# Kernel optimization log

Measured on AMD Instinct MI355X. Metric: run time of the kernel, lower is better.

Reference implementation:

```python
import jax, jax.numpy as jnp
import numpy as np

B, H, T = 32, 80, 1600
C1, C2 = 32, 32
K, S, P = 3, 2, 1  # kernel, stride, padding on both dims


def setup_inputs() -> dict:
    key = jax.random.key(0)
    k1, k2, k3, k4, k5, k6 = jax.random.split(key, 6)
    inputs = jax.random.normal(k1, (B, 1, H, T), dtype=jnp.float32)
    seq_lengths = jax.random.randint(k2, (B,), 1, T + 1).astype(jnp.int32)
    W1 = jax.random.normal(k3, (C1, 1, K, K), dtype=jnp.float32) * 0.1
    b1 = jax.random.normal(k4, (C1,), dtype=jnp.float32) * 0.1
    W2 = jax.random.normal(k5, (C2, C1, K, K), dtype=jnp.float32) * 0.05
    b2 = jax.random.normal(k6, (C2,), dtype=jnp.float32) * 0.1
    return {"inputs": inputs, "seq_lengths": seq_lengths,
            "W1": W1, "b1": b1, "W2": W2, "b2": b2}


def _conv(x, W, b):
    y = jax.lax.conv_general_dilated(
        x, W, window_strides=(S, S), padding=((P, P), (P, P)),
        dimension_numbers=("NCHW", "OIHW", "NCHW"))
    return y + b[None, :, None, None]


def _new_lengths(L):
    # floor((L + 2p - d*(k-1) - 1)/s) + 1, matching _get_sequence_lengths
    return (L + 2 * P - (K - 1) - 1) // S + 1


def _mask_time(x, L):
    # zero positions t >= L[b] along the last (time) axis
    t = jnp.arange(x.shape[3])
    valid = (t[None, :] < L[:, None]).astype(x.dtype)  # [B, Tout]
    return x * valid[:, None, None, :]


def reference(inputs, seq_lengths, W1, b1, W2, b2):
    # conv1 + mask
    x = _conv(inputs, W1, b1)
    L = _new_lengths(seq_lengths)
    x = _mask_time(x, L)
    # relu + mask (lengths unchanged)
    x = _mask_time(jax.nn.relu(x), L)
    # conv2 + mask
    x = _conv(x, W2, b2)
    L = _new_lengths(L)
    x = _mask_time(x, L)
    # relu + mask
    x = _mask_time(jax.nn.relu(x), L)
    return x, L
```

## Files before the change

### kernel.cpp

```cpp
#include <hip/hip_runtime.h>
#include <hip/hip_bf16.h>

#define B_    32
#define H_IN  80
#define T_IN  1600
#define C1_   32
#define H1_   40
#define T1_   800
#define C2_   32
#define H2_   20
#define T2_   400

#define TH2   2
#define TT2   32
#define NH1   5
#define NT1   65
#define NIDX  33
#define RROWS 11
#define RCOLSW 66
#define RWORDS (RROWS * RCOLSW)

#define NPOS   (NH1 * NT1)
#define NCHUNK 11

#define WS_W2FRAGS 1152
#define WS_W1OFF   1152
#define WS_TOTAL   1216
#define OUTN  (B_ * C2_ * H2_ * T2_)

#define OSTR  36

typedef unsigned int uint32;
typedef __attribute__((ext_vector_type(8)))  short short8;
typedef __attribute__((ext_vector_type(4)))  float f32x4;
typedef __attribute__((ext_vector_type(16))) float f32x16;
typedef __attribute__((ext_vector_type(2)))  uint32 u32x2;
typedef __attribute__((ext_vector_type(4)))  uint32 u32x4;

__device__ __forceinline__ unsigned short f2bf(float x) {
    __hip_bfloat16 h = __float2bfloat16(x);
    return __builtin_bit_cast(unsigned short, h);
}

__device__ __forceinline__ int x1off(int h1r, int t1r, int g) {
    int idx = t1r >> 1;
    int par = t1r & 1;
    return ((par * (NH1 * NIDX) + h1r * NIDX + idx) << 6) + (((g ^ idx) & 3) << 4);
}

__global__ void wprep(const float* __restrict__ W2, const float* __restrict__ W1,
                      const float* __restrict__ b1, unsigned short* __restrict__ ws) {
    int i = blockIdx.x * 256 + threadIdx.x;
    if (i < WS_W2FRAGS) {
        int mt   = i / 576;
        int rem  = i - mt * 576;
        int tap  = rem >> 6;
        int lane = rem & 63;
        int lg   = lane >> 4;
        int l15  = lane & 15;
        int c2   = mt * 16 + l15;
        short8 f;
#pragma unroll
        for (int j = 0; j < 8; ++j)
            f[j] = (short)f2bf(W2[((c2 * C1_) + lg * 8 + j) * 9 + tap]);
        *((short8*)ws + i) = f;
    } else if (i < WS_TOTAL) {
        int lane = i - WS_W1OFF;
        int c1 = lane & 31;
        int kb = (lane >> 5) * 8;
        short8 f;
#pragma unroll
        for (int j = 0; j < 8; ++j) {
            int k = kb + j;
            float v = (k < 9) ? W1[c1 * 9 + k] : (k == 9 ? b1[c1] : 0.0f);
            f[j] = (short)f2bf(v);
        }
        *((short8*)ws + i) = f;
    }
}

__global__ __launch_bounds__(256, 6) void fused_conv(
    const float* __restrict__ in, const int* __restrict__ seq,
    const float* __restrict__ b2,
    const unsigned short* __restrict__ ws,
    float* __restrict__ out)
{
    __shared__ __align__(16) char   x1mem[2 * NH1 * NIDX * 64];
    __shared__ __align__(16) uint32 raw32[RWORDS];

    const int tid  = threadIdx.x;
    const int lane = tid & 63;
    const int wv   = tid >> 6;
    const int l15  = lane & 15;
    const int lg   = lane >> 4;
    const int hi   = lane >> 5;
    const int n32  = lane & 31;
    const int b      = blockIdx.z;
    const int h2base = blockIdx.y * TH2;
    const int t2base = blockIdx.x * TT2;

    const int L  = seq[b];
    const int L1 = ((L  - 1) >> 1) + 1;
    const int L2 = ((L1 - 1) >> 1) + 1;

    if (blockIdx.x == 0 && blockIdx.y == 0 && tid == 0)
        out[OUTN + b] = (float)L2;

    if (t2base >= L2) {
        const f32x4 z4 = (f32x4){0.f, 0.f, 0.f, 0.f};
#pragma unroll
        for (int k = 0; k < 2; ++k) {
            int i = tid + k * 256;
            int row = i >> 3, q = i & 7;
            int c2 = row >> 1, r = row & 1;
            int t2g = t2base + 4 * q;
            if (t2g < T2_)
                __builtin_nontemporal_store(z4,
                    (f32x4*)(out + ((b * C2_ + c2) * H2_ + h2base + r) * T2_ + t2g));
        }
        return;
    }

    const int row0 = 4 * h2base - 3;
    const int t0   = 4 * t2base - 3;
    const float* inb = in + b * (H_IN * T_IN);
#pragma unroll
    for (int k = 0; k < 3; ++k) {
        int pi = tid + k * 256;
        if (pi < RWORDS) {
            int row = pi / RCOLSW;
            int q   = pi - row * RCOLSW;
            int h = row0 + row;
            int t = t0 + 2 * q;
            bool hok = (h >= 0) & (h < H_IN);
            bool ok0 = hok & (t >= 0) & (t < T_IN);
            bool ok1 = hok & (t + 1 >= 0) & (t + 1 < T_IN);
            float v0 = inb[ok0 ? h * T_IN + t     : 0];
            float v1 = inb[ok1 ? h * T_IN + t + 1 : 0];
            v0 = ok0 ? v0 : 0.0f;
            v1 = ok1 ? v1 : 0.0f;
            raw32[pi] = (uint32)f2bf(v0) | ((uint32)f2bf(v1) << 16);
        }
    }

    const short8 w1f = *((const short8*)ws + WS_W1OFF + lane);
    const int mt    = wv & 1;
    const int strip = wv >> 1;
    short8 afr[9];
#pragma unroll
    for (int tap = 0; tap < 9; ++tap)
        afr[tap] = *((const short8*)ws + (mt * 9 + tap) * 64 + lane);
    float b2r[4];
#pragma unroll
    for (int j = 0; j < 4; ++j) b2r[j] = b2[mt * 16 + lg * 4 + j];

    __syncthreads();

    const int h1base = 2 * h2base - 1;
    const int t1base = 2 * t2base - 1;
    for (int c = wv; c < NCHUNK; c += 4) {
        int p  = c * 32 + n32;
        int pc = p < NPOS ? p : NPOS - 1;
        int h1r = pc / NT1;
        int t1r = pc - h1r * NT1;

        const uint32* rp = raw32 + (2 * h1r) * RCOLSW + t1r;
        uint32 a0 = rp[0],            b0v = rp[1];
        uint32 a1 = rp[RCOLSW],       b1v = rp[RCOLSW + 1];
        uint32 a2 = rp[2 * RCOLSW],   b2v = rp[2 * RCOLSW + 1];

        uint32 w0l = a0;
        uint32 w1l = (b0v & 0xffffu) | (a1 << 16);
        uint32 w2l = (a1 >> 16) | (b1v << 16);
        uint32 w3l = a2;
        uint32 w0h = (b2v & 0xffffu) | 0x3f800000u;

        uint32 fw0 = hi ? w0h : w0l;
        uint32 fw1 = hi ? 0u  : w1l;
        uint32 fw2 = hi ? 0u  : w2l;
        uint32 fw3 = hi ? 0u  : w3l;
        short8 bfrag = __builtin_bit_cast(short8, (u32x4){fw0, fw1, fw2, fw3});

        f32x16 acc = {};
        acc = __builtin_amdgcn_mfma_f32_32x32x16_bf16(w1f, bfrag, acc, 0, 0, 0);

        int h1 = h1base + h1r;
        int t1 = t1base + t1r;
        bool okp = (h1 >= 0) && (t1 >= 0) && (t1 < L1);
        if (p < NPOS) {
#pragma unroll
            for (int g = 0; g < 4; ++g) {
                float v0 = okp ? fmaxf(acc[4 * g + 0], 0.0f) : 0.0f;
                float v1 = okp ? fmaxf(acc[4 * g + 1], 0.0f) : 0.0f;
                float v2 = okp ? fmaxf(acc[4 * g + 2], 0.0f) : 0.0f;
                float v3 = okp ? fmaxf(acc[4 * g + 3], 0.0f) : 0.0f;
                u32x2 dw;
                dw.x = (uint32)f2bf(v0) | ((uint32)f2bf(v1) << 16);
                dw.y = (uint32)f2bf(v2) | ((uint32)f2bf(v3) << 16);
                *(u32x2*)(x1mem + x1off(h1r, t1r, g) + hi * 8) = dw;
            }
        }
    }

    __syncthreads();

    f32x4 acc2[TH2];
#pragma unroll
    for (int r = 0; r < TH2; ++r) acc2[r] = (f32x4){0.f, 0.f, 0.f, 0.f};

#pragma unroll
    for (int tap = 0; tap < 9; ++tap) {
        const int kh = tap / 3;
        const int kt = tap % 3;
        const int t1r = 2 * (strip * 16 + l15) + kt;
#pragma unroll
        for (int r = 0; r < TH2; ++r) {
            short8 bx = *(const short8*)(x1mem + x1off(2 * r + kh, t1r, lg));
            acc2[r] = __builtin_amdgcn_mfma_f32_16x16x32_bf16(afr[tap], bx, acc2[r], 0, 0, 0);
        }
    }

    __syncthreads();

    float* obuf = (float*)x1mem;
    {
        const int t2 = t2base + strip * 16 + l15;
        const bool vm = (t2 < L2);
#pragma unroll
        for (int r = 0; r < TH2; ++r) {
#pragma unroll
            for (int j = 0; j < 4; ++j) {
                int c2 = mt * 16 + lg * 4 + j;
                float v = acc2[r][j] + b2r[j];
                v = vm ? fmaxf(v, 0.0f) : 0.0f;
                obuf[(c2 * TH2 + r) * OSTR + strip * 16 + l15] = v;
            }
        }
    }
    __syncthreads();

#pragma unroll
    for (int k = 0; k < 2; ++k) {
        int i = tid + k * 256;
        int row = i >> 3, q = i & 7;
        int c2 = row >> 1, r = row & 1;
        int t2g = t2base + 4 * q;
        f32x4 v = *(const f32x4*)(obuf + row * OSTR + 4 * q);
        if (t2g < T2_)
            __builtin_nontemporal_store(v,
                (f32x4*)(out + ((b * C2_ + c2) * H2_ + h2base + r) * T2_ + t2g));
    }
}

extern "C" void kernel_launch(void* const* d_in, const int* in_sizes, int n_in,
                              void* d_out, int out_size, void* d_ws, size_t ws_size,
                              hipStream_t stream) {
    const float* in  = (const float*)d_in[0];
    const int*   seq = (const int*)d_in[1];
    const float* W1  = (const float*)d_in[2];
    const float* b1  = (const float*)d_in[3];
    const float* W2  = (const float*)d_in[4];
    const float* b2  = (const float*)d_in[5];
    float* out = (float*)d_out;
    unsigned short* ws = (unsigned short*)d_ws;

    wprep<<<dim3((WS_TOTAL + 255) / 256), dim3(256), 0, stream>>>(W2, W1, b1, ws);

    dim3 grid((T2_ + TT2 - 1) / TT2, H2_ / TH2, B_);
    fused_conv<<<grid, dim3(256), 0, stream>>>(in, seq, b2, ws, out);
}
```

Baseline: 23.67 us.

## Fold weight-prep kernel into fused conv, converting weights to bf16 per block

```diff
diff --git a/kernel.cpp b/kernel.cpp
--- a/kernel.cpp
+++ b/kernel.cpp
@@ -22,10 +22,6 @@
 
 #define NPOS   (NH1 * NT1)
 #define NCHUNK 11
-
-#define WS_W2FRAGS 1152
-#define WS_W1OFF   1152
-#define WS_TOTAL   1216
 #define OUTN  (B_ * C2_ * H2_ * T2_)
 
 #define OSTR  36
@@ -48,41 +44,10 @@
     return ((par * (NH1 * NIDX) + h1r * NIDX + idx) << 6) + (((g ^ idx) & 3) << 4);
 }
 
-__global__ void wprep(const float* __restrict__ W2, const float* __restrict__ W1,
-                      const float* __restrict__ b1, unsigned short* __restrict__ ws) {
-    int i = blockIdx.x * 256 + threadIdx.x;
-    if (i < WS_W2FRAGS) {
-        int mt   = i / 576;
-        int rem  = i - mt * 576;
-        int tap  = rem >> 6;
-        int lane = rem & 63;
-        int lg   = lane >> 4;
-        int l15  = lane & 15;
-        int c2   = mt * 16 + l15;
-        short8 f;
-#pragma unroll
-        for (int j = 0; j < 8; ++j)
-            f[j] = (short)f2bf(W2[((c2 * C1_) + lg * 8 + j) * 9 + tap]);
-        *((short8*)ws + i) = f;
-    } else if (i < WS_TOTAL) {
-        int lane = i - WS_W1OFF;
-        int c1 = lane & 31;
-        int kb = (lane >> 5) * 8;
-        short8 f;
-#pragma unroll
-        for (int j = 0; j < 8; ++j) {
-            int k = kb + j;
-            float v = (k < 9) ? W1[c1 * 9 + k] : (k == 9 ? b1[c1] : 0.0f);
-            f[j] = (short)f2bf(v);
-        }
-        *((short8*)ws + i) = f;
-    }
-}
-
-__global__ __launch_bounds__(256, 6) void fused_conv(
+__global__ __launch_bounds__(256, 4) void fused_conv(
     const float* __restrict__ in, const int* __restrict__ seq,
-    const float* __restrict__ b2,
-    const unsigned short* __restrict__ ws,
+    const float* __restrict__ W1, const float* __restrict__ b1,
+    const float* __restrict__ W2, const float* __restrict__ b2,
     float* __restrict__ out)
 {
     __shared__ __align__(16) char   x1mem[2 * NH1 * NIDX * 64];
@@ -120,6 +85,41 @@
         }
         return;
     }
+
+    const int mt    = wv & 1;
+    const int strip = wv >> 1;
+
+    short8 afr[9];
+    {
+        const int c2 = mt * 16 + l15;
+        const f32x4* wp = (const f32x4*)(W2 + c2 * 288 + lg * 72);
+        f32x4 wb[18];
+#pragma unroll
+        for (int q = 0; q < 18; ++q) wb[q] = wp[q];
+        const float* wf = (const float*)wb;
+#pragma unroll
+        for (int tap = 0; tap < 9; ++tap) {
+            short8 f;
+#pragma unroll
+            for (int j = 0; j < 8; ++j)
+                f[j] = (short)f2bf(wf[j * 9 + tap]);
+            afr[tap] = f;
+        }
+    }
+
+    short8 w1f;
+    {
+        const float* w1r = W1 + n32 * 9;
+#pragma unroll
+        for (int j = 0; j < 8; ++j) {
+            int k = hi * 8 + j;
+            float v = (k < 9) ? w1r[k] : ((k == 9) ? b1[n32] : 0.0f);
+            w1f[j] = (short)f2bf(v);
+        }
+    }
+    float b2r[4];
+#pragma unroll
+    for (int j = 0; j < 4; ++j) b2r[j] = b2[mt * 16 + lg * 4 + j];
 
     const int row0 = 4 * h2base - 3;
     const int t0   = 4 * t2base - 3;
@@ -143,17 +143,6 @@
         }
     }
 
-    const short8 w1f = *((const short8*)ws + WS_W1OFF + lane);
-    const int mt    = wv & 1;
-    const int strip = wv >> 1;
-    short8 afr[9];
-#pragma unroll
-    for (int tap = 0; tap < 9; ++tap)
-        afr[tap] = *((const short8*)ws + (mt * 9 + tap) * 64 + lane);
-    float b2r[4];
-#pragma unroll
-    for (int j = 0; j < 4; ++j) b2r[j] = b2[mt * 16 + lg * 4 + j];
-
     __syncthreads();
 
     const int h1base = 2 * h2base - 1;
@@ -262,10 +251,7 @@
     const float* W2  = (const float*)d_in[4];
     const float* b2  = (const float*)d_in[5];
     float* out = (float*)d_out;
-    unsigned short* ws = (unsigned short*)d_ws;
-
-    wprep<<<dim3((WS_TOTAL + 255) / 256), dim3(256), 0, stream>>>(W2, W1, b1, ws);
 
     dim3 grid((T2_ + TT2 - 1) / TT2, H2_ / TH2, B_);
-    fused_conv<<<grid, dim3(256), 0, stream>>>(in, seq, b2, ws, out);
-}
+    fused_conv<<<grid, dim3(256), 0, stream>>>(in, seq, W1, b1, W2, b2, out);
+}
```

Result: slower. 39.54 us (+67.0%).

## Process two time tiles per block and prefetch next tile's input into registers

Applied to the files above, without the earlier changes.

```diff
diff --git a/kernel.cpp b/kernel.cpp
--- a/kernel.cpp
+++ b/kernel.cpp
@@ -79,54 +79,14 @@
     }
 }
 
-__global__ __launch_bounds__(256, 6) void fused_conv(
-    const float* __restrict__ in, const int* __restrict__ seq,
-    const float* __restrict__ b2,
-    const unsigned short* __restrict__ ws,
-    float* __restrict__ out)
-{
-    __shared__ __align__(16) char   x1mem[2 * NH1 * NIDX * 64];
-    __shared__ __align__(16) uint32 raw32[RWORDS];
-
-    const int tid  = threadIdx.x;
-    const int lane = tid & 63;
-    const int wv   = tid >> 6;
-    const int l15  = lane & 15;
-    const int lg   = lane >> 4;
-    const int hi   = lane >> 5;
-    const int n32  = lane & 31;
-    const int b      = blockIdx.z;
-    const int h2base = blockIdx.y * TH2;
-    const int t2base = blockIdx.x * TT2;
-
-    const int L  = seq[b];
-    const int L1 = ((L  - 1) >> 1) + 1;
-    const int L2 = ((L1 - 1) >> 1) + 1;
-
-    if (blockIdx.x == 0 && blockIdx.y == 0 && tid == 0)
-        out[OUTN + b] = (float)L2;
-
-    if (t2base >= L2) {
-        const f32x4 z4 = (f32x4){0.f, 0.f, 0.f, 0.f};
-#pragma unroll
-        for (int k = 0; k < 2; ++k) {
-            int i = tid + k * 256;
-            int row = i >> 3, q = i & 7;
-            int c2 = row >> 1, r = row & 1;
-            int t2g = t2base + 4 * q;
-            if (t2g < T2_)
-                __builtin_nontemporal_store(z4,
-                    (f32x4*)(out + ((b * C2_ + c2) * H2_ + h2base + r) * T2_ + t2g));
-        }
-        return;
-    }
-
+__device__ __forceinline__ void stage_load(const float* __restrict__ inb, int tid,
+                                           int h2base, int t2base, uint32 rv[3]) {
     const int row0 = 4 * h2base - 3;
     const int t0   = 4 * t2base - 3;
-    const float* inb = in + b * (H_IN * T_IN);
 #pragma unroll
     for (int k = 0; k < 3; ++k) {
         int pi = tid + k * 256;
+        uint32 v = 0u;
         if (pi < RWORDS) {
             int row = pi / RCOLSW;
             int q   = pi - row * RCOLSW;
@@ -139,9 +99,42 @@
             float v1 = inb[ok1 ? h * T_IN + t + 1 : 0];
             v0 = ok0 ? v0 : 0.0f;
             v1 = ok1 ? v1 : 0.0f;
-            raw32[pi] = (uint32)f2bf(v0) | ((uint32)f2bf(v1) << 16);
-        }
+            v = (uint32)f2bf(v0) | ((uint32)f2bf(v1) << 16);
+        }
+        rv[k] = v;
     }
+}
+
+__global__ __launch_bounds__(256, 6) void fused_conv(
+    const float* __restrict__ in, const int* __restrict__ seq,
+    const float* __restrict__ b2,
+    const unsigned short* __restrict__ ws,
+    float* __restrict__ out)
+{
+    __shared__ __align__(16) char   x1mem[2 * NH1 * NIDX * 64];
+    __shared__ __align__(16) uint32 raw32[RWORDS];
+
+    const int tid  = threadIdx.x;
+    const int lane = tid & 63;
+    const int wv   = tid >> 6;
+    const int l15  = lane & 15;
+    const int lg   = lane >> 4;
+    const int hi   = lane >> 5;
+    const int n32  = lane & 31;
+    const int b      = blockIdx.z;
+    const int h2base = blockIdx.y * TH2;
+    const int t2b0   = blockIdx.x * (2 * TT2);
+
+    const int L  = seq[b];
+    const int L1 = ((L  - 1) >> 1) + 1;
+    const int L2 = ((L1 - 1) >> 1) + 1;
+
+    if (blockIdx.x == 0 && blockIdx.y == 0 && tid == 0)
+        out[OUTN + b] = (float)L2;
+
+    const float* inb = in + b * (H_IN * T_IN);
+    const bool work0 = (t2b0 < L2);
+    const bool work1 = (t2b0 + TT2 < L2);
 
     const short8 w1f = *((const short8*)ws + WS_W1OFF + lane);
     const int mt    = wv & 1;
@@ -154,101 +147,132 @@
 #pragma unroll
     for (int j = 0; j < 4; ++j) b2r[j] = b2[mt * 16 + lg * 4 + j];
 
-    __syncthreads();
-
-    const int h1base = 2 * h2base - 1;
-    const int t1base = 2 * t2base - 1;
-    for (int c = wv; c < NCHUNK; c += 4) {
-        int p  = c * 32 + n32;
-        int pc = p < NPOS ? p : NPOS - 1;
-        int h1r = pc / NT1;
-        int t1r = pc - h1r * NT1;
-
-        const uint32* rp = raw32 + (2 * h1r) * RCOLSW + t1r;
-        uint32 a0 = rp[0],            b0v = rp[1];
-        uint32 a1 = rp[RCOLSW],       b1v = rp[RCOLSW + 1];
-        uint32 a2 = rp[2 * RCOLSW],   b2v = rp[2 * RCOLSW + 1];
-
-        uint32 w0l = a0;
-        uint32 w1l = (b0v & 0xffffu) | (a1 << 16);
-        uint32 w2l = (a1 >> 16) | (b1v << 16);
-        uint32 w3l = a2;
-        uint32 w0h = (b2v & 0xffffu) | 0x3f800000u;
-
-        uint32 fw0 = hi ? w0h : w0l;
-        uint32 fw1 = hi ? 0u  : w1l;
-        uint32 fw2 = hi ? 0u  : w2l;
-        uint32 fw3 = hi ? 0u  : w3l;
-        short8 bfrag = __builtin_bit_cast(short8, (u32x4){fw0, fw1, fw2, fw3});
-
-        f32x16 acc = {};
-        acc = __builtin_amdgcn_mfma_f32_32x32x16_bf16(w1f, bfrag, acc, 0, 0, 0);
-
-        int h1 = h1base + h1r;
-        int t1 = t1base + t1r;
-        bool okp = (h1 >= 0) && (t1 >= 0) && (t1 < L1);
-        if (p < NPOS) {
-#pragma unroll
-            for (int g = 0; g < 4; ++g) {
-                float v0 = okp ? fmaxf(acc[4 * g + 0], 0.0f) : 0.0f;
-                float v1 = okp ? fmaxf(acc[4 * g + 1], 0.0f) : 0.0f;
-                float v2 = okp ? fmaxf(acc[4 * g + 2], 0.0f) : 0.0f;
-                float v3 = okp ? fmaxf(acc[4 * g + 3], 0.0f) : 0.0f;
-                u32x2 dw;
-                dw.x = (uint32)f2bf(v0) | ((uint32)f2bf(v1) << 16);
-                dw.y = (uint32)f2bf(v2) | ((uint32)f2bf(v3) << 16);
-                *(u32x2*)(x1mem + x1off(h1r, t1r, g) + hi * 8) = dw;
-            }
-        }
-    }
-
-    __syncthreads();
-
-    f32x4 acc2[TH2];
-#pragma unroll
-    for (int r = 0; r < TH2; ++r) acc2[r] = (f32x4){0.f, 0.f, 0.f, 0.f};
-
-#pragma unroll
-    for (int tap = 0; tap < 9; ++tap) {
-        const int kh = tap / 3;
-        const int kt = tap % 3;
-        const int t1r = 2 * (strip * 16 + l15) + kt;
-#pragma unroll
-        for (int r = 0; r < TH2; ++r) {
-            short8 bx = *(const short8*)(x1mem + x1off(2 * r + kh, t1r, lg));
-            acc2[r] = __builtin_amdgcn_mfma_f32_16x16x32_bf16(afr[tap], bx, acc2[r], 0, 0, 0);
-        }
-    }
-
-    __syncthreads();
-
-    float* obuf = (float*)x1mem;
-    {
-        const int t2 = t2base + strip * 16 + l15;
-        const bool vm = (t2 < L2);
-#pragma unroll
-        for (int r = 0; r < TH2; ++r) {
-#pragma unroll
-            for (int j = 0; j < 4; ++j) {
-                int c2 = mt * 16 + lg * 4 + j;
-                float v = acc2[r][j] + b2r[j];
-                v = vm ? fmaxf(v, 0.0f) : 0.0f;
-                obuf[(c2 * TH2 + r) * OSTR + strip * 16 + l15] = v;
-            }
-        }
-    }
-    __syncthreads();
-
-#pragma unroll
-    for (int k = 0; k < 2; ++k) {
-        int i = tid + k * 256;
-        int row = i >> 3, q = i & 7;
-        int c2 = row >> 1, r = row & 1;
-        int t2g = t2base + 4 * q;
-        f32x4 v = *(const f32x4*)(obuf + row * OSTR + 4 * q);
-        if (t2g < T2_)
-            __builtin_nontemporal_store(v,
-                (f32x4*)(out + ((b * C2_ + c2) * H2_ + h2base + r) * T2_ + t2g));
+    uint32 rv[3];
+    if (work0)      stage_load(inb, tid, h2base, t2b0, rv);
+    else if (work1) stage_load(inb, tid, h2base, t2b0 + TT2, rv);
+
+#pragma unroll
+    for (int tt = 0; tt < 2; ++tt) {
+        const int t2base = t2b0 + tt * TT2;
+        const bool workT = tt == 0 ? work0 : work1;
+
+        if (!workT) {
+            const f32x4 z4 = (f32x4){0.f, 0.f, 0.f, 0.f};
+#pragma unroll
+            for (int k = 0; k < 2; ++k) {
+                int i = tid + k * 256;
+                int row = i >> 3, q = i & 7;
+                int c2 = row >> 1, r = row & 1;
+                int t2g = t2base + 4 * q;
+                if (t2g < T2_)
+                    __builtin_nontemporal_store(z4,
+                        (f32x4*)(out + ((b * C2_ + c2) * H2_ + h2base + r) * T2_ + t2g));
+            }
+            continue;
+        }
+
+#pragma unroll
+        for (int k = 0; k < 3; ++k) {
+            int pi = tid + k * 256;
+            if (pi < RWORDS) raw32[pi] = rv[k];
+        }
+        __syncthreads();
+
+        const int h1base = 2 * h2base - 1;
+        const int t1base = 2 * t2base - 1;
+        for (int c = wv; c < NCHUNK; c += 4) {
+            int p  = c * 32 + n32;
+            int pc = p < NPOS ? p : NPOS - 1;
+            int h1r = pc / NT1;
+            int t1r = pc - h1r * NT1;
+
+            const uint32* rp = raw32 + (2 * h1r) * RCOLSW + t1r;
+            uint32 a0 = rp[0],            b0v = rp[1];
+            uint32 a1 = rp[RCOLSW],       b1v = rp[RCOLSW + 1];
+            uint32 a2 = rp[2 * RCOLSW],   b2v = rp[2 * RCOLSW + 1];
+
+            uint32 w0l = a0;
+            uint32 w1l = (b0v & 0xffffu) | (a1 << 16);
+            uint32 w2l = (a1 >> 16) | (b1v << 16);
+            uint32 w3l = a2;
+            uint32 w0h = (b2v & 0xffffu) | 0x3f800000u;
+
+            uint32 fw0 = hi ? w0h : w0l;
+            uint32 fw1 = hi ? 0u  : w1l;
+            uint32 fw2 = hi ? 0u  : w2l;
+            uint32 fw3 = hi ? 0u  : w3l;
+            short8 bfrag = __builtin_bit_cast(short8, (u32x4){fw0, fw1, fw2, fw3});
+
+            f32x16 acc = {};
+            acc = __builtin_amdgcn_mfma_f32_32x32x16_bf16(w1f, bfrag, acc, 0, 0, 0);
+
+            int h1 = h1base + h1r;
+            int t1 = t1base + t1r;
+            bool okp = (h1 >= 0) && (t1 >= 0) && (t1 < L1);
+            if (p < NPOS) {
+#pragma unroll
+                for (int g = 0; g < 4; ++g) {
+                    float v0 = okp ? fmaxf(acc[4 * g + 0], 0.0f) : 0.0f;
+                    float v1 = okp ? fmaxf(acc[4 * g + 1], 0.0f) : 0.0f;
+                    float v2 = okp ? fmaxf(acc[4 * g + 2], 0.0f) : 0.0f;
+                    float v3 = okp ? fmaxf(acc[4 * g + 3], 0.0f) : 0.0f;
+                    u32x2 dw;
+                    dw.x = (uint32)f2bf(v0) | ((uint32)f2bf(v1) << 16);
+                    dw.y = (uint32)f2bf(v2) | ((uint32)f2bf(v3) << 16);
+                    *(u32x2*)(x1mem + x1off(h1r, t1r, g) + hi * 8) = dw;
+                }
+            }
+        }
+        __syncthreads();
+
+        if (tt == 0 && work1)
+            stage_load(inb, tid, h2base, t2b0 + TT2, rv);
+
+        f32x4 acc2[TH2];
+#pragma unroll
+        for (int r = 0; r < TH2; ++r) acc2[r] = (f32x4){0.f, 0.f, 0.f, 0.f};
+
+#pragma unroll
+        for (int tap = 0; tap < 9; ++tap) {
+            const int kh = tap / 3;
+            const int kt = tap % 3;
+            const int t1r = 2 * (strip * 16 + l15) + kt;
+#pragma unroll
+            for (int r = 0; r < TH2; ++r) {
+                short8 bx = *(const short8*)(x1mem + x1off(2 * r + kh, t1r, lg));
+                acc2[r] = __builtin_amdgcn_mfma_f32_16x16x32_bf16(afr[tap], bx, acc2[r], 0, 0, 0);
+            }
+        }
+        __syncthreads();
+
+        float* obuf = (float*)x1mem;
+        {
+            const int t2 = t2base + strip * 16 + l15;
+            const bool vm = (t2 < L2);
+#pragma unroll
+            for (int r = 0; r < TH2; ++r) {
+#pragma unroll
+                for (int j = 0; j < 4; ++j) {
+                    int c2 = mt * 16 + lg * 4 + j;
+                    float v = acc2[r][j] + b2r[j];
+                    v = vm ? fmaxf(v, 0.0f) : 0.0f;
+                    obuf[(c2 * TH2 + r) * OSTR + strip * 16 + l15] = v;
+                }
+            }
+        }
+        __syncthreads();
+
+#pragma unroll
+        for (int k = 0; k < 2; ++k) {
+            int i = tid + k * 256;
+            int row = i >> 3, q = i & 7;
+            int c2 = row >> 1, r = row & 1;
+            int t2g = t2base + 4 * q;
+            f32x4 v = *(const f32x4*)(obuf + row * OSTR + 4 * q);
+            if (t2g < T2_)
+                __builtin_nontemporal_store(v,
+                    (f32x4*)(out + ((b * C2_ + c2) * H2_ + h2base + r) * T2_ + t2g));
+        }
     }
 }
 
@@ -266,6 +290,6 @@
 
     wprep<<<dim3((WS_TOTAL + 255) / 256), dim3(256), 0, stream>>>(W2, W1, b1, ws);
 
-    dim3 grid((T2_ + TT2 - 1) / TT2, H2_ / TH2, B_);
+    dim3 grid(7, H2_ / TH2, B_);
     fused_conv<<<grid, dim3(256), 0, stream>>>(in, seq, b2, ws, out);
 }
```

Result: slower. 31.30 us (+32.2%).
